# Performance work log

Measured on AMD Instinct MI355X. Metric: run time of the kernel, lower is better.

Reference implementation:

```python
import jax, jax.numpy as jnp
import numpy as np

# ---- static SO(3) metadata: 128 channels for each l in {0,1,2,3} ----
NCL = 128
LMAX = 3
METADATA = [NCL] * (LMAX + 1)
NC = sum(METADATA)                      # 512 total channels (onebody MLP width)
REP = sum((2 * l + 1) * NCL for l in range(LMAX + 1))  # 2048 rep components
D = REP // 4                            # folded dim (stride=4)
N = 64                                  # batch (nodes)

# channel index of every rep component; layout per l is m-major, channels contiguous
_offsets = np.cumsum([0] + METADATA[:-1])
_CIND = np.concatenate([
    np.tile(np.arange(_offsets[l], _offsets[l] + METADATA[l]), 2 * l + 1)
    for l in range(LMAX + 1)
])
CIND = jnp.asarray(_CIND)  # [REP] int32

NORM_EPS = 1e-2   # RepNorm gauge divisor eps
BN_EPS = 1e-5     # BatchNorm1d eps


def swish(x):
    return x * jax.nn.sigmoid(x)


def setup_inputs() -> dict:
    key = jax.random.key(0)
    ks = jax.random.split(key, 10)
    return {
        "x1d": jax.random.normal(ks[0], (N, REP), jnp.float32),
        "x2d": jax.random.normal(ks[1], (N, D, D, 4), jnp.float32),
        "W1": jax.random.normal(ks[2], (NC, NC), jnp.float32) / np.float32(np.sqrt(NC)),
        "b1": jnp.zeros((NC,), jnp.float32),
        "W2": jax.random.normal(ks[3], (NC, NC), jnp.float32) / np.float32(np.sqrt(NC)),
        "b2": jnp.zeros((NC,), jnp.float32),
        "Wie": jax.random.normal(ks[4], (LMAX + 1, NCL, NCL), jnp.float32) / np.float32(np.sqrt(NCL)),
        "Wt": jax.random.normal(ks[5], (4, 4), jnp.float32) * np.float32(0.5),
        "Wg": jax.random.normal(ks[6], (4, 4), jnp.float32) * np.float32(0.5),
        "bg": jnp.zeros((4,), jnp.float32),
    }


def reference(x1d, x2d, W1, b1, W2, b2, Wie, Wt, Wg, bg):
    # ---- RepNorm1d: invariant per-(l,channel) L2 norm over m, batchnorm, gauge ----
    norm = jnp.sqrt(jax.ops.segment_sum((x1d * x1d).T, CIND, num_segments=NC).T)  # [N, NC]
    mu = norm.mean(axis=0)
    var = ((norm - mu) ** 2).mean(axis=0)
    n = (norm - mu) / jnp.sqrt(var + BN_EPS)          # BatchNorm1d (gamma=1, beta=0, train stats)
    g = x1d / (norm[:, CIND] + NORM_EPS)              # gauge tensor [N, REP]

    # ---- onebody MLP on invariants ----
    n = swish(n @ W1.T + b1) @ W2.T + b2              # [N, NC]

    # ---- IELin: per-degree channel mixing (applied identically across m) ----
    outs = []
    off = 0
    for l in range(LMAX + 1):
        width = (2 * l + 1) * NCL
        blk = g[:, off:off + width].reshape(-1, 2 * l + 1, NCL)
        outs.append(jnp.einsum('nmi,oi->nmo', blk, Wie[l]).reshape(blk.shape[0], width))
        off += width
    g = jnp.concatenate(outs, axis=-1)                # [N, REP]

    # ---- scalar_mul: broadcast invariant scalars over m within each channel ----
    x1d_new = g * n[:, CIND]                          # [N, REP]

    # ---- fold(stride=4) and twobody gated bilinear contraction ----
    f = x1d_new.reshape(-1, D, 4)                     # [N, D, 4]
    a = jnp.einsum('npqc,nqc->npc', x2d, f)           # contract q  -> [N, D, 4]
    a = jnp.einsum('npc,npc->nc', a, f)               # contract p  -> [N, 4]
    a = swish(a @ Wg.T + bg)                          # twobody gate [N, 4]

    x2d_new = jnp.einsum('npqc,dc->npqd', x2d, Wt) * a[:, None, None, :]  # [N, D, D, 4]
    return (x1d_new, x2d_new)
```

## Files before the change

kernel.cpp:

```cpp
#include <hip/hip_runtime.h>
#include <math.h>

#define Nn   64
#define NCL_ 128
#define NCc  512
#define REPr 2048
#define Dd   512

__device__ __forceinline__ float swishf(float x) { return x * (1.0f / (1.0f + __expf(-x))); }

__global__ void k_norm(const float* __restrict__ x1d, float* __restrict__ norm,
                       float* __restrict__ a2) {
    int n = blockIdx.x;
    int c = threadIdx.x;
    int l = c >> 7;
    int ch = c & 127;
    int off = l * l * 128;
    int nm = 2 * l + 1;
    const float* base = x1d + n * REPr + off + ch;
    float s = 0.f;
    for (int m = 0; m < nm; m++) { float v = base[m * 128]; s += v * v; }
    norm[n * NCc + c] = sqrtf(s);
    if (blockIdx.x == 0 && c < Nn * 4) a2[c] = 0.f;
}

__global__ void k_bn(const float* __restrict__ norm, float* __restrict__ nb) {
    int c = threadIdx.x;
    float s = 0.f, s2 = 0.f;
    for (int n = 0; n < Nn; n++) { float v = norm[n * NCc + c]; s += v; s2 += v * v; }
    float mu = s * (1.0f / Nn);
    float var = s2 * (1.0f / Nn) - mu * mu;
    float inv = rsqrtf(var + 1e-5f);
    for (int n = 0; n < Nn; n++) nb[n * NCc + c] = (norm[n * NCc + c] - mu) * inv;
}

__global__ void k_dense(const float* __restrict__ in, const float* __restrict__ W,
                        const float* __restrict__ b, float* __restrict__ out, int act) {
    int wave = blockIdx.x * 4 + (threadIdx.x >> 6);
    int lane = threadIdx.x & 63;
    int n = wave >> 6;
    int j0 = (wave & 63) * 8;
    float xv[8];
#pragma unroll
    for (int k = 0; k < 8; k++) xv[k] = in[n * NCc + k * 64 + lane];
#pragma unroll
    for (int jj = 0; jj < 8; jj++) {
        int j = j0 + jj;
        const float* row = W + j * NCc;
        float acc = 0.f;
#pragma unroll
        for (int k = 0; k < 8; k++) acc += xv[k] * row[k * 64 + lane];
        for (int m = 1; m < 64; m <<= 1) acc += __shfl_xor(acc, m, 64);
        if (lane == 0) {
            float y = acc + b[j];
            out[n * NCc + j] = act ? swishf(y) : y;
        }
    }
}

__global__ void k_ielin(const float* __restrict__ x1d, const float* __restrict__ norm,
                        const float* __restrict__ n2, const float* __restrict__ Wie,
                        float* __restrict__ out) {
    __shared__ float gv[NCL_];
    int bid = blockIdx.x;
    int n = bid >> 4;
    int lm = bid & 15;
    int l = (lm >= 9) ? 3 : ((lm >= 4) ? 2 : ((lm >= 1) ? 1 : 0));
    int off = lm * 128;
    int coff = l * 128;
    int t = threadIdx.x;
    gv[t] = x1d[n * REPr + off + t] / (norm[n * NCc + coff + t] + 1e-2f);
    __syncthreads();
    const float* wrow = Wie + l * NCL_ * NCL_ + t * NCL_;
    float acc = 0.f;
    for (int i = 0; i < NCL_; i++) acc += gv[i] * wrow[i];
    out[n * REPr + off + t] = acc * n2[n * NCc + coff + t];
}

__global__ void k_bilinear(const float* __restrict__ x2d, const float* __restrict__ f,
                           float* __restrict__ a2) {
    __shared__ float4 fbuf[Dd];
    __shared__ float cont[4][4];
    int bid = blockIdx.x;
    int n = bid >> 7;
    int pg = bid & 127;
    int tid = threadIdx.x;
    const float4* f4 = (const float4*)(f + n * REPr);
    fbuf[tid] = f4[tid];
    fbuf[tid + 256] = f4[tid + 256];
    __syncthreads();
    int w = tid >> 6, lane = tid & 63;
    int p = pg * 4 + w;
    const float4* x4 = (const float4*)x2d + (size_t)(n * Dd + p) * Dd;
    float4 acc = {0.f, 0.f, 0.f, 0.f};
    for (int q = lane; q < Dd; q += 64) {
        float4 xv = x4[q];
        float4 fv = fbuf[q];
        acc.x += xv.x * fv.x; acc.y += xv.y * fv.y;
        acc.z += xv.z * fv.z; acc.w += xv.w * fv.w;
    }
    for (int m = 1; m < 64; m <<= 1) {
        acc.x += __shfl_xor(acc.x, m, 64);
        acc.y += __shfl_xor(acc.y, m, 64);
        acc.z += __shfl_xor(acc.z, m, 64);
        acc.w += __shfl_xor(acc.w, m, 64);
    }
    if (lane == 0) {
        float4 fp = fbuf[p];
        cont[w][0] = acc.x * fp.x; cont[w][1] = acc.y * fp.y;
        cont[w][2] = acc.z * fp.z; cont[w][3] = acc.w * fp.w;
    }
    __syncthreads();
    if (tid < 4) {
        float s = cont[0][tid] + cont[1][tid] + cont[2][tid] + cont[3][tid];
        atomicAdd(&a2[n * 4 + tid], s);
    }
}

__global__ void k_out2d(const float* __restrict__ x2d, const float* __restrict__ a2,
                        const float* __restrict__ Wt, const float* __restrict__ Wg,
                        const float* __restrict__ bg, float* __restrict__ out) {
    int bid = blockIdx.x;
    int n = bid >> 6;
    int chunk = bid & 63;
    float a[4], gate[4], sw[16];
#pragma unroll
    for (int c = 0; c < 4; c++) a[c] = a2[n * 4 + c];
#pragma unroll
    for (int d = 0; d < 4; d++) {
        float y = bg[d];
#pragma unroll
        for (int c = 0; c < 4; c++) y += Wg[d * 4 + c] * a[c];
        gate[d] = swishf(y);
    }
#pragma unroll
    for (int d = 0; d < 4; d++)
#pragma unroll
        for (int c = 0; c < 4; c++) sw[d * 4 + c] = Wt[d * 4 + c] * gate[d];
    const float4* in4 = (const float4*)x2d;
    float4* out4 = (float4*)out;
    size_t base = (size_t)n * (Dd * Dd) + (size_t)chunk * 4096 + threadIdx.x;
#pragma unroll
    for (int i = 0; i < 16; i++) {
        size_t e = base + (size_t)i * 256;
        float4 x = in4[e];
        float4 y;
        y.x = sw[0] * x.x + sw[1] * x.y + sw[2] * x.z + sw[3] * x.w;
        y.y = sw[4] * x.x + sw[5] * x.y + sw[6] * x.z + sw[7] * x.w;
        y.z = sw[8] * x.x + sw[9] * x.y + sw[10] * x.z + sw[11] * x.w;
        y.w = sw[12] * x.x + sw[13] * x.y + sw[14] * x.z + sw[15] * x.w;
        out4[e] = y;
    }
}

extern "C" void kernel_launch(void* const* d_in, const int* in_sizes, int n_in,
                              void* d_out, int out_size, void* d_ws, size_t ws_size,
                              hipStream_t stream) {
    const float* x1d = (const float*)d_in[0];
    const float* x2d = (const float*)d_in[1];
    const float* W1  = (const float*)d_in[2];
    const float* b1  = (const float*)d_in[3];
    const float* W2  = (const float*)d_in[4];
    const float* b2  = (const float*)d_in[5];
    const float* Wie = (const float*)d_in[6];
    const float* Wt  = (const float*)d_in[7];
    const float* Wg  = (const float*)d_in[8];
    const float* bg  = (const float*)d_in[9];

    float* out1d = (float*)d_out;
    float* out2d = out1d + (size_t)Nn * REPr;

    float* ws   = (float*)d_ws;
    float* norm = ws;
    float* nb   = ws + 32768;
    float* h    = ws + 65536;
    float* n2   = ws + 98304;
    float* a2   = ws + 131072;

    k_norm<<<Nn, NCc, 0, stream>>>(x1d, norm, a2);
    k_bn<<<1, NCc, 0, stream>>>(norm, nb);
    k_dense<<<1024, 256, 0, stream>>>(nb, W1, b1, h, 1);
    k_dense<<<1024, 256, 0, stream>>>(h, W2, b2, n2, 0);
    k_ielin<<<Nn * 16, NCL_, 0, stream>>>(x1d, norm, n2, Wie, out1d);
    k_bilinear<<<Nn * 128, 256, 0, stream>>>(x2d, out1d, a2);
    k_out2d<<<Nn * 64, 256, 0, stream>>>(x2d, a2, Wt, Wg, bg, out2d);
}
```

Baseline: 543.5 us.

## Chunk bilinear/out2d by node groups for cache reuse, fuse norm+BN, transpose Wie

```diff
diff --git a/kernel.cpp b/kernel.cpp
--- a/kernel.cpp
+++ b/kernel.cpp
@@ -9,29 +9,46 @@
 
 __device__ __forceinline__ float swishf(float x) { return x * (1.0f / (1.0f + __expf(-x))); }
 
-__global__ void k_norm(const float* __restrict__ x1d, float* __restrict__ norm,
-                       float* __restrict__ a2) {
-    int n = blockIdx.x;
-    int c = threadIdx.x;
+__global__ void k_normbn(const float* __restrict__ x1d, float* __restrict__ norm,
+                         float* __restrict__ nb, float* __restrict__ a2) {
+    int c = blockIdx.x;
+    int n = threadIdx.x;
     int l = c >> 7;
     int ch = c & 127;
-    int off = l * l * 128;
     int nm = 2 * l + 1;
-    const float* base = x1d + n * REPr + off + ch;
+    const float* base = x1d + n * REPr + l * l * 128 + ch;
     float s = 0.f;
     for (int m = 0; m < nm; m++) { float v = base[m * 128]; s += v * v; }
-    norm[n * NCc + c] = sqrtf(s);
-    if (blockIdx.x == 0 && c < Nn * 4) a2[c] = 0.f;
-}
-
-__global__ void k_bn(const float* __restrict__ norm, float* __restrict__ nb) {
-    int c = threadIdx.x;
-    float s = 0.f, s2 = 0.f;
-    for (int n = 0; n < Nn; n++) { float v = norm[n * NCc + c]; s += v; s2 += v * v; }
-    float mu = s * (1.0f / Nn);
+    float nv = sqrtf(s);
+    float s1 = nv, s2 = nv * nv;
+    for (int m = 1; m < 64; m <<= 1) {
+        s1 += __shfl_xor(s1, m, 64);
+        s2 += __shfl_xor(s2, m, 64);
+    }
+    float mu  = s1 * (1.0f / Nn);
     float var = s2 * (1.0f / Nn) - mu * mu;
     float inv = rsqrtf(var + 1e-5f);
-    for (int n = 0; n < Nn; n++) nb[n * NCc + c] = (norm[n * NCc + c] - mu) * inv;
+    norm[n * NCc + c] = nv;
+    nb[n * NCc + c]   = (nv - mu) * inv;
+    if (c < 4) a2[c * 64 + n] = 0.f;
+}
+
+__global__ void k_twie(const float* __restrict__ Wie, float* __restrict__ WieT) {
+    __shared__ float t[32][33];
+    int l  = blockIdx.x >> 4;
+    int tb = blockIdx.x & 15;
+    int ro = (tb >> 2) * 32;
+    int ci = (tb & 3) * 32;
+    int tx = threadIdx.x & 31, ty = threadIdx.x >> 5;
+    const float* src = Wie  + l * 16384;
+    float*       dst = WieT + l * 16384;
+#pragma unroll
+    for (int k = 0; k < 32; k += 8)
+        t[ty + k][tx] = src[(ro + ty + k) * 128 + ci + tx];
+    __syncthreads();
+#pragma unroll
+    for (int k = 0; k < 32; k += 8)
+        dst[(ci + ty + k) * 128 + ro + tx] = t[tx][ty + k];
 }
 
 __global__ void k_dense(const float* __restrict__ in, const float* __restrict__ W,
@@ -40,16 +57,17 @@
     int lane = threadIdx.x & 63;
     int n = wave >> 6;
     int j0 = (wave & 63) * 8;
-    float xv[8];
-#pragma unroll
-    for (int k = 0; k < 8; k++) xv[k] = in[n * NCc + k * 64 + lane];
+    const float4* in4 = (const float4*)(in + n * NCc);
+    float4 xa = in4[lane * 2];
+    float4 xb = in4[lane * 2 + 1];
 #pragma unroll
     for (int jj = 0; jj < 8; jj++) {
         int j = j0 + jj;
-        const float* row = W + j * NCc;
-        float acc = 0.f;
-#pragma unroll
-        for (int k = 0; k < 8; k++) acc += xv[k] * row[k * 64 + lane];
+        const float4* row = (const float4*)(W + j * NCc);
+        float4 wa = row[lane * 2];
+        float4 wb = row[lane * 2 + 1];
+        float acc = xa.x * wa.x + xa.y * wa.y + xa.z * wa.z + xa.w * wa.w
+                  + xb.x * wb.x + xb.y * wb.y + xb.z * wb.z + xb.w * wb.w;
         for (int m = 1; m < 64; m <<= 1) acc += __shfl_xor(acc, m, 64);
         if (lane == 0) {
             float y = acc + b[j];
@@ -59,7 +77,7 @@
 }
 
 __global__ void k_ielin(const float* __restrict__ x1d, const float* __restrict__ norm,
-                        const float* __restrict__ n2, const float* __restrict__ Wie,
+                        const float* __restrict__ n2, const float* __restrict__ WieT,
                         float* __restrict__ out) {
     __shared__ float gv[NCL_];
     int bid = blockIdx.x;
@@ -71,18 +89,19 @@
     int t = threadIdx.x;
     gv[t] = x1d[n * REPr + off + t] / (norm[n * NCc + coff + t] + 1e-2f);
     __syncthreads();
-    const float* wrow = Wie + l * NCL_ * NCL_ + t * NCL_;
+    const float* w = WieT + l * NCL_ * NCL_;
     float acc = 0.f;
-    for (int i = 0; i < NCL_; i++) acc += gv[i] * wrow[i];
+#pragma unroll 8
+    for (int i = 0; i < NCL_; i++) acc += gv[i] * w[i * NCL_ + t];
     out[n * REPr + off + t] = acc * n2[n * NCc + coff + t];
 }
 
 __global__ void k_bilinear(const float* __restrict__ x2d, const float* __restrict__ f,
-                           float* __restrict__ a2) {
+                           float* __restrict__ a2, int n0) {
     __shared__ float4 fbuf[Dd];
     __shared__ float cont[4][4];
     int bid = blockIdx.x;
-    int n = bid >> 7;
+    int n = n0 + (bid >> 7);
     int pg = bid & 127;
     int tid = threadIdx.x;
     const float4* f4 = (const float4*)(f + n * REPr);
@@ -119,9 +138,9 @@
 
 __global__ void k_out2d(const float* __restrict__ x2d, const float* __restrict__ a2,
                         const float* __restrict__ Wt, const float* __restrict__ Wg,
-                        const float* __restrict__ bg, float* __restrict__ out) {
+                        const float* __restrict__ bg, float* __restrict__ out, int n0) {
     int bid = blockIdx.x;
-    int n = bid >> 6;
+    int n = n0 + (bid >> 6);
     int chunk = bid & 63;
     float a[4], gate[4], sw[16];
 #pragma unroll
@@ -176,12 +195,15 @@
     float* h    = ws + 65536;
     float* n2   = ws + 98304;
     float* a2   = ws + 131072;
-
-    k_norm<<<Nn, NCc, 0, stream>>>(x1d, norm, a2);
-    k_bn<<<1, NCc, 0, stream>>>(norm, nb);
+    float* WieT = ws + 131328;
+
+    k_normbn<<<NCc, 64, 0, stream>>>(x1d, norm, nb, a2);
+    k_twie<<<64, 256, 0, stream>>>(Wie, WieT);
     k_dense<<<1024, 256, 0, stream>>>(nb, W1, b1, h, 1);
     k_dense<<<1024, 256, 0, stream>>>(h, W2, b2, n2, 0);
-    k_ielin<<<Nn * 16, NCL_, 0, stream>>>(x1d, norm, n2, Wie, out1d);
-    k_bilinear<<<Nn * 128, 256, 0, stream>>>(x2d, out1d, a2);
-    k_out2d<<<Nn * 64, 256, 0, stream>>>(x2d, a2, Wt, Wg, bg, out2d);
-}
+    k_ielin<<<Nn * 16, NCL_, 0, stream>>>(x1d, norm, n2, WieT, out1d);
+    for (int g = 0; g < 8; g++) {
+        k_bilinear<<<8 * 128, 256, 0, stream>>>(x2d, out1d, a2, g * 8);
+        k_out2d<<<8 * 64, 256, 0, stream>>>(x2d, a2, Wt, Wg, bg, out2d, g * 8);
+    }
+}
```

Result: slower. 576.0 us (+6.0%).
